# Kernel optimization log

Measured on AMD Instinct MI355X. Metric: run time of the kernel, lower is better.

## Reference

```python
import jax, jax.numpy as jnp
import numpy as np

ACT = jax.nn.relu
REG = 1.0  # semi_dual_sgd passes reg=1 (not self.e)
N_ITER = 1000


def _convt(x, w, b, out_pad):
    # PyTorch ConvTranspose2d, w layout [Cin, Cout, kh, kw], k=3, stride=2, padding=1
    wk = jnp.transpose(w[:, :, ::-1, ::-1], (1, 0, 2, 3))  # -> OIHW
    y = jax.lax.conv_general_dilated(
        x, wk, window_strides=(1, 1),
        padding=((1, 1 + out_pad), (1, 1 + out_pad)),
        lhs_dilation=(2, 2),
        dimension_numbers=("NCHW", "OIHW", "NCHW"))
    return y + b[None, :, None, None]


def _conv(x, w, b):
    # Conv2d k=3, padding=1, w layout OIHW
    y = jax.lax.conv_general_dilated(
        x, w, window_strides=(1, 1), padding=((1, 1), (1, 1)),
        dimension_numbers=("NCHW", "OIHW", "NCHW"))
    return y + b[None, :, None, None]


def _decoder_logits(z, fc_w, fc_b, ct0_w, ct0_b, ct1_w, ct1_b, fct_w, fct_b, conv_w, conv_b):
    h = ACT(z @ fc_w + fc_b)            # [n, 128*16]
    h = h.reshape(-1, 128, 4, 4)
    h = ACT(_convt(h, ct0_w, ct0_b, 0))  # [n, 64, 7, 7]  (img_size==28 branch: output_padding=0)
    h = ACT(_convt(h, ct1_w, ct1_b, 1))  # [n, 32, 14, 14]
    h = ACT(_convt(h, fct_w, fct_b, 1))  # [n, 32, 28, 28]
    return _conv(h, conv_w, conv_b)      # [n, 1, 28, 28] Bernoulli logits


def _cost_matrix(x, logit):
    # C[i,j] = -sum_pix Bernoulli(logits=logit_j).log_prob(x_i)
    # log_prob = x*logit - softplus(logit); sum over pixels factorizes into a GEMM.
    B = x.shape[0]
    n = logit.shape[0]
    X = x.reshape(B, -1)          # [B, P]
    L = logit.reshape(n, -1)      # [n, P]
    sp = jnp.sum(jax.nn.softplus(L), axis=1)  # [n]
    return -(X @ L.T) + sp[None, :]           # [B, n]


def _sag_semi_dual(C, idx, reg):
    # SAG on the semi-dual entropic OT objective (Genevay et al. / POT-style),
    # uniform marginals, lr = reg / max(a) = reg * n_src.
    n_src, n_tgt = C.shape
    a = jnp.full((n_src,), 1.0 / n_src, dtype=C.dtype)
    b = jnp.full((n_tgt,), 1.0 / n_tgt, dtype=C.dtype)
    log_b = jnp.log(b)
    lr = reg * n_src

    def step(carry, i):
        beta, stored, ssum = carry
        # stable softmax form of exp(-(C[i]-beta)/reg)*b / sum(...)
        khi = jax.nn.softmax((beta - C[i]) / reg + log_b)
        g = a[i] * (b - khi)
        ssum = ssum + g - stored[i]
        stored = stored.at[i].set(g)
        beta = beta + (lr / n_src) * ssum
        return (beta, stored, ssum), None

    init = (jnp.zeros((n_tgt,), C.dtype), jnp.zeros((n_src, n_tgt), C.dtype), jnp.zeros((n_tgt,), C.dtype))
    (beta, _, _), _ = jax.lax.scan(step, init, idx)

    # entropic c-transform and primal plan recovery
    alpha = -reg * jax.scipy.special.logsumexp((beta[None, :] - C) / reg + log_b[None, :], axis=1)
    P = jnp.exp((alpha[:, None] + beta[None, :] - C) / reg) * a[:, None] * b[None, :]
    return P, a, b


def _omega(x):
    xs = jnp.where(x <= 0.0, 1.0, x)
    return jnp.sum(xs * jnp.log(xs))


def setup_inputs() -> dict:
    key = jax.random.key(0)
    ks = jax.random.split(key, 16)
    B, N, LAT = 512, 512, 64
    s = 0.05
    return {
        "x": jax.random.uniform(ks[0], (B, 1, 28, 28), jnp.float32),
        "z": jax.random.normal(ks[1], (N, LAT), jnp.float32),
        "fc_w": jax.random.normal(ks[2], (LAT, 128 * 16), jnp.float32) * s,
        "fc_b": jnp.zeros((128 * 16,), jnp.float32),
        "ct0_w": jax.random.normal(ks[3], (128, 64, 3, 3), jnp.float32) * s,
        "ct0_b": jnp.zeros((64,), jnp.float32),
        "ct1_w": jax.random.normal(ks[4], (64, 32, 3, 3), jnp.float32) * s,
        "ct1_b": jnp.zeros((32,), jnp.float32),
        "fct_w": jax.random.normal(ks[5], (32, 32, 3, 3), jnp.float32) * s,
        "fct_b": jnp.zeros((32,), jnp.float32),
        "conv_w": jax.random.normal(ks[6], (1, 32, 3, 3), jnp.float32) * s,
        "conv_b": jnp.zeros((1,), jnp.float32),
        "idx": jax.random.randint(ks[7], (N_ITER,), 0, B, jnp.int32),
    }


def reference(x, z, fc_w, fc_b, ct0_w, ct0_b, ct1_w, ct1_b, fct_w, fct_b, conv_w, conv_b, idx):
    logit = _decoder_logits(z, fc_w, fc_b, ct0_w, ct0_b, ct1_w, ct1_b, fct_w, fct_b, conv_w, conv_b)
    C = _cost_matrix(x, logit)                 # [B, n_sample]
    P, px, pz = _sag_semi_dual(C, idx, REG)    # numItermax=1000, reg=1
    kl = _omega(P) - _omega(px) - _omega(pz)
    return (P, C, kl)
```

## Files before the change

### kernel.cpp

```cpp
#include <hip/hip_runtime.h>
#include <hip/hip_bf16.h>
#include <math.h>


typedef float vf4 __attribute__((ext_vector_type(4)));

__global__ void fc_relu_k(const float* __restrict__ z, const float* __restrict__ w,
                          const float* __restrict__ b, float* __restrict__ out) {
  int n = blockIdx.x >> 1;
  int c0 = ((blockIdx.x & 1) << 10) + threadIdx.x * 4;
  const float* zr = z + n * 64;
  float4 acc = *(const float4*)&b[c0];
#pragma unroll
  for (int k = 0; k < 64; ++k) {
    float zk = zr[k];
    float4 wv = *(const float4*)&w[k * 2048 + c0];
    acc.x = fmaf(zk, wv.x, acc.x);
    acc.y = fmaf(zk, wv.y, acc.y);
    acc.z = fmaf(zk, wv.z, acc.z);
    acc.w = fmaf(zk, wv.w, acc.w);
  }
  acc.x = fmaxf(acc.x, 0.f); acc.y = fmaxf(acc.y, 0.f);
  acc.z = fmaxf(acc.z, 0.f); acc.w = fmaxf(acc.w, 0.f);
  *(float4*)&out[n * 2048 + c0] = acc;
}

#define TAPF(T, P, XV) { \
  const float4* w4_ = reinterpret_cast<const float4*>(&wt[((T) * CIN + ci) * 8]); \
  float4 wa_ = w4_[0], wb_ = w4_[1]; \
  acc[P][0] = fmaf(XV, wa_.x, acc[P][0]); \
  acc[P][1] = fmaf(XV, wa_.y, acc[P][1]); \
  acc[P][2] = fmaf(XV, wa_.z, acc[P][2]); \
  acc[P][3] = fmaf(XV, wa_.w, acc[P][3]); \
  acc[P][4] = fmaf(XV, wb_.x, acc[P][4]); \
  acc[P][5] = fmaf(XV, wb_.y, acc[P][5]); \
  acc[P][6] = fmaf(XV, wb_.z, acc[P][6]); \
  acc[P][7] = fmaf(XV, wb_.w, acc[P][7]); }

template <int CIN, int COUT, int HIN, int HOUT>
__global__ void convt_quad_k(const float* __restrict__ x, const float* __restrict__ w,
                             const float* __restrict__ bias, float* __restrict__ y) {
  constexpr bool FULL = (HOUT == 2 * HIN);
  constexpr int QP = HIN * HIN;
  __shared__ float wt[9 * CIN * 8];
  const int tid = threadIdx.x;
  const int g8 = blockIdx.y * 8;
  for (int e = tid; e < 9 * CIN * 8; e += 256) {
    int cl = e & 7;
    int rest = e >> 3;
    int ci = rest & (CIN - 1);
    int t = rest / CIN;
    wt[e] = w[((size_t)ci * COUT + g8 + cl) * 9 + t];
  }
  __syncthreads();

  int q = blockIdx.x * 256 + tid;
  int n = q / QP;
  int pq = q % QP;
  int a = pq / HIN, b = pq % HIN;
  const bool oka = (a + 1 < HIN), okb = (b + 1 < HIN);
  const float* xim = x + (size_t)n * CIN * QP + a * HIN + b;

  float acc[4][8];
#pragma unroll
  for (int p = 0; p < 4; ++p)
#pragma unroll
    for (int c = 0; c < 8; ++c) acc[p][c] = 0.f;

  for (int ci = 0; ci < CIN; ++ci) {
    const float* xc = xim + ci * QP;
    float x00 = xc[0];
    float x01 = okb ? xc[1] : 0.f;
    float x10 = oka ? xc[HIN] : 0.f;
    float x11 = (oka && okb) ? xc[HIN + 1] : 0.f;
    TAPF(4, 0, x00)
    TAPF(3, 1, x01) TAPF(5, 1, x00)
    TAPF(1, 2, x10) TAPF(7, 2, x00)
    TAPF(0, 3, x11) TAPF(2, 3, x10) TAPF(6, 3, x01) TAPF(8, 3, x00)
  }

  int oh0 = 2 * a, ow0 = 2 * b;
  bool vh = FULL || (oh0 + 1 < HOUT);
  bool vw = FULL || (ow0 + 1 < HOUT);
#pragma unroll
  for (int c = 0; c < 8; ++c) {
    float bv = bias[g8 + c];
    float o00 = fmaxf(acc[0][c] + bv, 0.f);
    float o01 = fmaxf(acc[1][c] + bv, 0.f);
    float o10 = fmaxf(acc[2][c] + bv, 0.f);
    float o11 = fmaxf(acc[3][c] + bv, 0.f);
    float* yb = y + (((size_t)n * COUT + g8 + c) * HOUT + oh0) * (size_t)HOUT + ow0;
    if (FULL) {
      *(float2*)yb = make_float2(o00, o01);
      *(float2*)(yb + HOUT) = make_float2(o10, o11);
    } else {
      yb[0] = o00;
      if (vw) yb[1] = o01;
      if (vh) yb[HOUT] = o10;
      if (vh && vw) yb[HOUT + 1] = o11;
    }
  }
}

__global__ void conv_final_k(const float* __restrict__ x, const float* __restrict__ w,
                             const float* __restrict__ bias, float* __restrict__ y) {
  __shared__ float ws_[288];
  int tid = threadIdx.x;
  if (tid < 288) ws_[tid] = w[tid];
  __syncthreads();
  int gid = blockIdx.x * 256 + tid;
  int ow = gid % 28;
  int t1 = gid / 28;
  int oh = t1 % 28;
  int n = t1 / 28;
  bool h0 = oh > 0, h2 = oh < 27, w0 = ow > 0, w2 = ow < 27;
  const float* xb = x + (size_t)n * 32 * 784 + (oh - 1) * 28 + (ow - 1);
  float acc = bias[0];
  for (int ci = 0; ci < 32; ++ci) {
    const float* xc = xb + ci * 784;
    const float* wc = &ws_[ci * 9];
    if (h0 && w0) acc = fmaf(xc[0], wc[0], acc);
    if (h0)       acc = fmaf(xc[1], wc[1], acc);
    if (h0 && w2) acc = fmaf(xc[2], wc[2], acc);
    if (w0)       acc = fmaf(xc[28], wc[3], acc);
                  acc = fmaf(xc[29], wc[4], acc);
    if (w2)       acc = fmaf(xc[30], wc[5], acc);
    if (h2 && w0) acc = fmaf(xc[56], wc[6], acc);
    if (h2)       acc = fmaf(xc[57], wc[7], acc);
    if (h2 && w2) acc = fmaf(xc[58], wc[8], acc);
  }
  y[gid] = acc;
}

template <int CTRL>
__device__ __forceinline__ float dpp_f(float x) {
  return __int_as_float(__builtin_amdgcn_update_dpp(0, __float_as_int(x), CTRL, 0xF, 0xF, true));
}
__device__ __forceinline__ float rdl(float v, int l) {
  return __int_as_float(__builtin_amdgcn_readlane(__float_as_int(v), l));
}
__device__ __forceinline__ float wsum64_l63(float v) {
  v += dpp_f<0xB1>(v);
  v += dpp_f<0x4E>(v);
  v += dpp_f<0x141>(v);
  v += dpp_f<0x140>(v);
  v += dpp_f<0x142>(v);
  v += dpp_f<0x143>(v);
  return rdl(v, 63);
}
__device__ __forceinline__ float wmax64_l63(float v) {
  v = fmaxf(v, dpp_f<0xB1>(v));
  v = fmaxf(v, dpp_f<0x4E>(v));
  v = fmaxf(v, dpp_f<0x141>(v));
  v = fmaxf(v, dpp_f<0x140>(v));
  v = fmaxf(v, dpp_f<0x142>(v));
  v = fmaxf(v, dpp_f<0x143>(v));
  return rdl(v, 63);
}

__global__ void cost_k(const float* __restrict__ X, const float* __restrict__ L,
                       float* __restrict__ Craw, float* __restrict__ sp) {
  __shared__ float Xs[16][36];
  __shared__ float Ls[16][68];
  int tid = threadIdx.x;
  int i0 = blockIdx.y * 32, j0 = blockIdx.x * 64;
  int lrow = tid >> 2;
  int lq = tid & 3;
  int xrow = tid & 31;
  int xq = (tid >> 5) & 3;
  bool doX = tid < 128;
  bool doSP = (blockIdx.y == 0);
  int tx = tid & 15, ty = tid >> 4;
  float acc[2][4] = {};
  float spacc = 0.f;
  for (int k0 = 0; k0 < 784; k0 += 16) {
    float4 lv = *(const float4*)&L[(size_t)(j0 + lrow) * 784 + k0 + lq * 4];
    float4 xv = {0.f, 0.f, 0.f, 0.f};
    if (doX) xv = *(const float4*)&X[(size_t)(i0 + xrow) * 784 + k0 + xq * 4];
    __syncthreads();
    Ls[lq * 4 + 0][lrow] = lv.x; Ls[lq * 4 + 1][lrow] = lv.y;
    Ls[lq * 4 + 2][lrow] = lv.z; Ls[lq * 4 + 3][lrow] = lv.w;
    if (doX) {
      Xs[xq * 4 + 0][xrow] = xv.x; Xs[xq * 4 + 1][xrow] = xv.y;
      Xs[xq * 4 + 2][xrow] = xv.z; Xs[xq * 4 + 3][xrow] = xv.w;
    }
    if (doSP) {
      spacc += fmaxf(lv.x, 0.f) + log1pf(__expf(-fabsf(lv.x)));
      spacc += fmaxf(lv.y, 0.f) + log1pf(__expf(-fabsf(lv.y)));
      spacc += fmaxf(lv.z, 0.f) + log1pf(__expf(-fabsf(lv.z)));
      spacc += fmaxf(lv.w, 0.f) + log1pf(__expf(-fabsf(lv.w)));
    }
    __syncthreads();
#pragma unroll
    for (int k = 0; k < 16; ++k) {
      float2 a = *(const float2*)&Xs[k][ty * 2];
      float4 bq = *(const float4*)&Ls[k][tx * 4];
      acc[0][0] = fmaf(a.x, bq.x, acc[0][0]); acc[0][1] = fmaf(a.x, bq.y, acc[0][1]);
      acc[0][2] = fmaf(a.x, bq.z, acc[0][2]); acc[0][3] = fmaf(a.x, bq.w, acc[0][3]);
      acc[1][0] = fmaf(a.y, bq.x, acc[1][0]); acc[1][1] = fmaf(a.y, bq.y, acc[1][1]);
      acc[1][2] = fmaf(a.y, bq.z, acc[1][2]); acc[1][3] = fmaf(a.y, bq.w, acc[1][3]);
    }
  }
#pragma unroll
  for (int r = 0; r < 2; ++r) {
    float4 o = make_float4(acc[r][0], acc[r][1], acc[r][2], acc[r][3]);
    *(float4*)&Craw[(size_t)(i0 + ty * 2 + r) * 512 + j0 + tx * 4] = o;
  }
  if (doSP) {
    float q = spacc;
    q += dpp_f<0xB1>(q);
    q += dpp_f<0x4E>(q);
    if (lq == 0) sp[j0 + lrow] = q;
  }
}

__global__ void prep_k(const float* __restrict__ craw, const float* __restrict__ sp,
                       float* __restrict__ D2) {
  __shared__ float red[256];
  int i = blockIdx.x, tid = threadIdx.x;
  float c0 = craw[(size_t)i * 512 + tid];
  float c1 = craw[(size_t)i * 512 + tid + 256];
  float v0 = c0 - sp[tid];
  float v1 = c1 - sp[tid + 256];
  red[tid] = fmaxf(v0, v1);
  __syncthreads();
  for (int st = 128; st > 0; st >>= 1) {
    if (tid < st) red[tid] = fmaxf(red[tid], red[tid + st]);
    __syncthreads();
  }
  float m = red[0];
  const float L2E = 1.4426950408889634f;
  D2[(size_t)i * 512 + tid] = (m - v0) * L2E;
  D2[(size_t)i * 512 + tid + 256] = (m - v1) * L2E;
}

#define SLD0(ROW) { const float* cp_ = D2 + ((size_t)(unsigned)(ROW) << 9) + jb; \
  s0dA = *(const vf4*)cp_; s0dB = *(const vf4*)(cp_ + 4); \
  const float* tp_ = stored + ((size_t)(unsigned)(ROW) << 9) + jb; \
  s0sA = *(const vf4*)tp_; s0sB = *(const vf4*)(tp_ + 4); }
#define SLD1(ROW) { const float* cp_ = D2 + ((size_t)(unsigned)(ROW) << 9) + jb; \
  s1dA = *(const vf4*)cp_; s1dB = *(const vf4*)(cp_ + 4); \
  const float* tp_ = stored + ((size_t)(unsigned)(ROW) << 9) + jb; \
  s1sA = *(const vf4*)tp_; s1sB = *(const vf4*)(tp_ + 4); }

#define STEP(RR, PFR, DA, DB, SA, SB, LDM, \
             R1,A1,B1, R2,A2,B2, R3,A3,B3, R4,A4,B4, R5,A5,B5, R6,A6,B6, \
             GA, GB) \
{ \
  vf4 d0_ = DA, d1_ = DB, t0_ = SA, t1_ = SB; \
  LDM(PFR); \
  const int r_ = (RR); \
  if (__builtin_expect((r_==(R1)) | (r_==(R2)) | (r_==(R3)) | \
                       (r_==(R4)) | (r_==(R5)) | (r_==(R6)), 0)) { \
    if (r_==(R6)) { t0_ = A6; t1_ = B6; } \
    if (r_==(R5)) { t0_ = A5; t1_ = B5; } \
    if (r_==(R4)) { t0_ = A4; t1_ = B4; } \
    if (r_==(R3)) { t0_ = A3; t1_ = B3; } \
    if (r_==(R2)) { t0_ = A2; t1_ = B2; } \
    if (r_==(R1)) { t0_ = A1; t1_ = B1; } \
  } \
  vf4 u0_ = ssumL - t0_; \
  vf4 u1_ = ssumH - t1_; \
  vf4 a0_ = betaL - d0_; \
  vf4 a1_ = betaH - d1_; \
  vf4 e0_, e1_; \
  e0_.x = __builtin_amdgcn_exp2f(a0_.x); e0_.y = __builtin_amdgcn_exp2f(a0_.y); \
  e0_.z = __builtin_amdgcn_exp2f(a0_.z); e0_.w = __builtin_amdgcn_exp2f(a0_.w); \
  e1_.x = __builtin_amdgcn_exp2f(a1_.x); e1_.y = __builtin_amdgcn_exp2f(a1_.y); \
  e1_.z = __builtin_amdgcn_exp2f(a1_.z); e1_.w = __builtin_amdgcn_exp2f(a1_.w); \
  vf4 es_ = e0_ + e1_; \
  float S_ = wsum64_l63((es_.x + es_.z) + (es_.y + es_.w)); \
  S_ = fmaxf(S_, 1e-35f); \
  float kk_ = C2NL * __builtin_amdgcn_rcpf(S_); \
  vf4 g0_ = e0_ * kk_ + c1l4; \
  vf4 g1_ = e1_ * kk_ + c1l4; \
  ssumL = u0_ + g0_; ssumH = u1_ + g1_; \
  betaL += ssumL; betaH += ssumH; \
  float* wp_ = stored + ((size_t)(unsigned)r_ << 9) + jb; \
  *(vf4*)wp_ = g0_; *(vf4*)(wp_ + 4) = g1_; \
  GA = g0_; GB = g1_; \
}

__global__ void __launch_bounds__(512, 1) sag_k(const float* __restrict__ D2,
                                                const int* __restrict__ idx,
                                                float* __restrict__ stored,
                                                float* __restrict__ beta_out) {
  const int tid = threadIdx.x;
  if (tid >= 64) {
    const vf4* c4 = (const vf4*)D2;
    const vf4* s4 = (const vf4*)stored;
    vf4 acc = {0.f, 0.f, 0.f, 0.f};
    for (int p = tid - 64; p < 65536; p += 448) { acc += c4[p]; acc += s4[p]; }
    float accs = acc.x + acc.y + acc.z + acc.w;
    asm volatile("" :: "v"(accs));
    return;
  }

  const int jb = tid * 8;
  const float C2NL = -0.0028177637f;
  const vf4 c1l4 = {5.503574e-06f, 5.503574e-06f, 5.503574e-06f, 5.503574e-06f};

  vf4 z4 = {0.f, 0.f, 0.f, 0.f};
  vf4 betaL = z4, betaH = z4, ssumL = z4, ssumH = z4;
  vf4 h1A = z4, h1B = z4, h2A = z4, h2B = z4, h3A = z4, h3B = z4;
  vf4 h4A = z4, h4B = z4, h5A = z4, h5B = z4, h6A = z4, h6B = z4;
  int hr1 = -1, hr2 = -1, hr3 = -1, hr4 = -1, hr5 = -1, hr6 = -1;
  float vsh = 0.f;

  int4 ia = *(const int4*)&idx[0];
  int4 ib = *(const int4*)&idx[4];
  int i0 = ia.x, i1 = ia.y, i2 = ia.z, i3 = ia.w;
  int i4 = ib.x, i5 = ib.y, i6 = ib.z, i7 = ib.w;

  vf4 s0dA, s0dB, s0sA, s0sB, s1dA, s1dB, s1sA, s1sB;
  SLD0(i0);
  SLD1(i1);

  vf4 g0a, g0b, g1a, g1b, g2a, g2b, g3a, g3b;
  vf4 g4a, g4b, g5a, g5b, g6a, g6b, g7a, g7b;

  for (int t = 0; t < 1000; t += 8) {
    int tb = (t + 8 < 1000) ? (t + 8) : 992;
    int4 na = *(const int4*)&idx[tb];
    int4 nb = *(const int4*)&idx[tb + 4];

    STEP(i0, i2, s0dA, s0dB, s0sA, s0sB, SLD0,
         hr1,h1A,h1B, hr2,h2A,h2B, hr3,h3A,h3B, hr4,h4A,h4B, hr5,h5A,h5B, hr6,h6A,h6B,
         g0a, g0b)
    STEP(i1, i3, s1dA, s1dB, s1sA, s1sB, SLD1,
         i0,g0a,g0b, hr1,h1A,h1B, hr2,h2A,h2B, hr3,h3A,h3B, hr4,h4A,h4B, hr5,h5A,h5B,
         g1a, g1b)
    STEP(i2, i4, s0dA, s0dB, s0sA, s0sB, SLD0,
         i1,g1a,g1b, i0,g0a,g0b, hr1,h1A,h1B, hr2,h2A,h2B, hr3,h3A,h3B, hr4,h4A,h4B,
         g2a, g2b)
    STEP(i3, i5, s1dA, s1dB, s1sA, s1sB, SLD1,
         i2,g2a,g2b, i1,g1a,g1b, i0,g0a,g0b, hr1,h1A,h1B, hr2,h2A,h2B, hr3,h3A,h3B,
         g3a, g3b)
    STEP(i4, i6, s0dA, s0dB, s0sA, s0sB, SLD0,
         i3,g3a,g3b, i2,g2a,g2b, i1,g1a,g1b, i0,g0a,g0b, hr1,h1A,h1B, hr2,h2A,h2B,
         g4a, g4b)
    STEP(i5, i7, s1dA, s1dB, s1sA, s1sB, SLD1,
         i4,g4a,g4b, i3,g3a,g3b, i2,g2a,g2b, i1,g1a,g1b, i0,g0a,g0b, hr1,h1A,h1B,
         g5a, g5b)
    STEP(i6, na.x, s0dA, s0dB, s0sA, s0sB, SLD0,
         i5,g5a,g5b, i4,g4a,g4b, i3,g3a,g3b, i2,g2a,g2b, i1,g1a,g1b, i0,g0a,g0b,
         g6a, g6b)
    STEP(i7, na.y, s1dA, s1dB, s1sA, s1sB, SLD1,
         i6,g6a,g6b, i5,g5a,g5b, i4,g4a,g4b, i3,g3a,g3b, i2,g2a,g2b, i1,g1a,g1b,
         g7a, g7b)

    {
      vf4 qm;
      qm.x = fmaxf(betaL.x, betaH.x); qm.y = fmaxf(betaL.y, betaH.y);
      qm.z = fmaxf(betaL.z, betaH.z); qm.w = fmaxf(betaL.w, betaH.w);
      float lm = fmaxf(fmaxf(qm.x, qm.y), fmaxf(qm.z, qm.w));
      float dm = wmax64_l63(lm);
      betaL = betaL - dm; betaH = betaH - dm;
      vsh += dm;
    }

    hr1 = i7; h1A = g7a; h1B = g7b;
    hr2 = i6; h2A = g6a; h2B = g6b;
    hr3 = i5; h3A = g5a; h3B = g5b;
    hr4 = i4; h4A = g4a; h4B = g4b;
    hr5 = i3; h5A = g3a; h5B = g3b;
    hr6 = i2; h6A = g2a; h6B = g2b;
    i0 = na.x; i1 = na.y; i2 = na.z; i3 = na.w;
    i4 = nb.x; i5 = nb.y; i6 = nb.z; i7 = nb.w;
  }

  const float LN2 = 0.6931471805599453f;
  vf4 oL = (betaL + vsh) * LN2;
  vf4 oH = (betaH + vsh) * LN2;
  *(vf4*)(beta_out + jb) = oL;
  *(vf4*)(beta_out + jb + 4) = oH;
}

__global__ void p_k(const float* __restrict__ craw, const float* __restrict__ sp,
                    const float* __restrict__ beta, float* __restrict__ P,
                    float* __restrict__ Cout, float* __restrict__ rowsum) {
  __shared__ float red[256];
  int i = blockIdx.x, tid = threadIdx.x;
  float c0 = craw[(size_t)i * 512 + tid];
  float c1 = craw[(size_t)i * 512 + tid + 256];
  float sp0 = sp[tid], sp1 = sp[tid + 256];
  float u0 = (beta[tid] - sp0) + c0;
  float u1 = (beta[tid + 256] - sp1) + c1;
  Cout[(size_t)i * 512 + tid] = sp0 - c0;
  Cout[(size_t)i * 512 + tid + 256] = sp1 - c1;
  float m = fmaxf(u0, u1);
  red[tid] = m;
  __syncthreads();
  for (int st = 128; st > 0; st >>= 1) {
    if (tid < st) red[tid] = fmaxf(red[tid], red[tid + st]);
    __syncthreads();
  }
  m = red[0];
  __syncthreads();
  float e0 = __expf(u0 - m), e1 = __expf(u1 - m);
  red[tid] = e0 + e1;
  __syncthreads();
  for (int st = 128; st > 0; st >>= 1) {
    if (tid < st) red[tid] += red[tid + st];
    __syncthreads();
  }
  float lse = m + logf(red[0]);
  __syncthreads();
  const float log512 = 6.238324625039508f;
  float p0 = __expf(u0 - lse) * (1.0f / 512.0f);
  float p1 = __expf(u1 - lse) * (1.0f / 512.0f);
  P[(size_t)i * 512 + tid] = p0;
  P[(size_t)i * 512 + tid + 256] = p1;
  float pl = p0 * (u0 - lse - log512) + p1 * (u1 - lse - log512);
  red[tid] = pl;
  __syncthreads();
  for (int st = 128; st > 0; st >>= 1) {
    if (tid < st) red[tid] += red[tid + st];
    __syncthreads();
  }
  if (tid == 0) rowsum[i] = red[0];
}

__global__ void kl_k(const float* __restrict__ rowsum, float* __restrict__ out_kl) {
  __shared__ float red[512];
  int tid = threadIdx.x;
  red[tid] = rowsum[tid];
  __syncthreads();
  for (int st = 256; st > 0; st >>= 1) {
    if (tid < st) red[tid] += red[tid + st];
    __syncthreads();
  }
  if (tid == 0) out_kl[0] = red[0] + 2.0f * 6.238324625039508f;
}

extern "C" void kernel_launch(void* const* d_in, const int* in_sizes, int n_in,
                              void* d_out, int out_size, void* d_ws, size_t ws_size,
                              hipStream_t stream) {
  const float* x = (const float*)d_in[0];
  const float* z = (const float*)d_in[1];
  const float* fc_w = (const float*)d_in[2];
  const float* fc_b = (const float*)d_in[3];
  const float* ct0_w = (const float*)d_in[4];
  const float* ct0_b = (const float*)d_in[5];
  const float* ct1_w = (const float*)d_in[6];
  const float* ct1_b = (const float*)d_in[7];
  const float* fct_w = (const float*)d_in[8];
  const float* fct_b = (const float*)d_in[9];
  const float* conv_w = (const float*)d_in[10];
  const float* conv_b = (const float*)d_in[11];
  const int* idx = (const int*)d_in[12];

  float* out = (float*)d_out;
  float* Pout = out;
  float* Cout = out + 262144;
  float* klout = out + 524288;

  float* ws = (float*)d_ws;
  float* h0 = ws;
  float* h1 = h0 + 1048576;
  float* h2 = h1 + 1605632;
  float* h3 = h2 + 3211264;
  float* logit = h3 + 12845056;
  float* sp = logit + 401408;
  float* beta = sp + 512;
  float* stored = beta + 512;
  float* rowsum = stored + 262144;
  float* Craw = h0;
  float* D2 = h1;

  hipMemsetAsync(stored, 0, 262144 * sizeof(float), stream);

  fc_relu_k<<<1024, 256, 0, stream>>>(z, fc_w, fc_b, h0);
  convt_quad_k<128, 64, 4, 7><<<dim3(32, 8), 256, 0, stream>>>(h0, ct0_w, ct0_b, h1);
  convt_quad_k<64, 32, 7, 14><<<dim3(98, 4), 256, 0, stream>>>(h1, ct1_w, ct1_b, h2);
  convt_quad_k<32, 32, 14, 28><<<dim3(392, 4), 256, 0, stream>>>(h2, fct_w, fct_b, h3);
  conv_final_k<<<1568, 256, 0, stream>>>(h3, conv_w, conv_b, logit);
  cost_k<<<dim3(8, 16), 256, 0, stream>>>(x, logit, Craw, sp);
  prep_k<<<512, 256, 0, stream>>>(Craw, sp, D2);
  sag_k<<<1, 512, 0, stream>>>(D2, idx, stored, beta);
  p_k<<<512, 256, 0, stream>>>(Craw, sp, beta, Pout, Cout, rowsum);
  kl_k<<<1, 512, 0, stream>>>(rowsum, klout);
}
```

Measured before the change: 540.3 us.

## Split SAG loop across eight waves, one column per lane, LDS reduction

```diff
diff --git a/kernel.cpp b/kernel.cpp
--- a/kernel.cpp
+++ b/kernel.cpp
@@ -234,146 +234,107 @@
   D2[(size_t)i * 512 + tid + 256] = (m - v1) * L2E;
 }
 
-#define SLD0(ROW) { const float* cp_ = D2 + ((size_t)(unsigned)(ROW) << 9) + jb; \
-  s0dA = *(const vf4*)cp_; s0dB = *(const vf4*)(cp_ + 4); \
-  const float* tp_ = stored + ((size_t)(unsigned)(ROW) << 9) + jb; \
-  s0sA = *(const vf4*)tp_; s0sB = *(const vf4*)(tp_ + 4); }
-#define SLD1(ROW) { const float* cp_ = D2 + ((size_t)(unsigned)(ROW) << 9) + jb; \
-  s1dA = *(const vf4*)cp_; s1dB = *(const vf4*)(cp_ + 4); \
-  const float* tp_ = stored + ((size_t)(unsigned)(ROW) << 9) + jb; \
-  s1sA = *(const vf4*)tp_; s1sB = *(const vf4*)(tp_ + 4); }
-
-#define STEP(RR, PFR, DA, DB, SA, SB, LDM, \
-             R1,A1,B1, R2,A2,B2, R3,A3,B3, R4,A4,B4, R5,A5,B5, R6,A6,B6, \
-             GA, GB) \
+#define SPF(SLOTD, SLOTS, ROW) { unsigned ro_ = (unsigned)(ROW); \
+  SLOTD = D2[((size_t)ro_ << 9) + col]; \
+  SLOTS = stored[((size_t)ro_ << 9) + col]; }
+
+#define SSTEP(RR, PFR, SD, SS, PAR, R1,G1, R2,G2, R3,G3, R4,G4, R5,G5, R6,G6, GOUT) \
 { \
-  vf4 d0_ = DA, d1_ = DB, t0_ = SA, t1_ = SB; \
-  LDM(PFR); \
+  float d_ = SD, st_ = SS; \
+  SPF(SD, SS, PFR) \
   const int r_ = (RR); \
   if (__builtin_expect((r_==(R1)) | (r_==(R2)) | (r_==(R3)) | \
                        (r_==(R4)) | (r_==(R5)) | (r_==(R6)), 0)) { \
-    if (r_==(R6)) { t0_ = A6; t1_ = B6; } \
-    if (r_==(R5)) { t0_ = A5; t1_ = B5; } \
-    if (r_==(R4)) { t0_ = A4; t1_ = B4; } \
-    if (r_==(R3)) { t0_ = A3; t1_ = B3; } \
-    if (r_==(R2)) { t0_ = A2; t1_ = B2; } \
-    if (r_==(R1)) { t0_ = A1; t1_ = B1; } \
+    if (r_==(R6)) st_ = G6; \
+    if (r_==(R5)) st_ = G5; \
+    if (r_==(R4)) st_ = G4; \
+    if (r_==(R3)) st_ = G3; \
+    if (r_==(R2)) st_ = G2; \
+    if (r_==(R1)) st_ = G1; \
   } \
-  vf4 u0_ = ssumL - t0_; \
-  vf4 u1_ = ssumH - t1_; \
-  vf4 a0_ = betaL - d0_; \
-  vf4 a1_ = betaH - d1_; \
-  vf4 e0_, e1_; \
-  e0_.x = __builtin_amdgcn_exp2f(a0_.x); e0_.y = __builtin_amdgcn_exp2f(a0_.y); \
-  e0_.z = __builtin_amdgcn_exp2f(a0_.z); e0_.w = __builtin_amdgcn_exp2f(a0_.w); \
-  e1_.x = __builtin_amdgcn_exp2f(a1_.x); e1_.y = __builtin_amdgcn_exp2f(a1_.y); \
-  e1_.z = __builtin_amdgcn_exp2f(a1_.z); e1_.w = __builtin_amdgcn_exp2f(a1_.w); \
-  vf4 es_ = e0_ + e1_; \
-  float S_ = wsum64_l63((es_.x + es_.z) + (es_.y + es_.w)); \
+  float e_ = __builtin_amdgcn_exp2f(beta - d_); \
+  float part_ = wsum64_l63(e_); \
+  if (lane == 63) sdata[(PAR) * 8 + wid] = part_; \
+  __syncthreads(); \
+  vf4 qa_ = *(const vf4*)&sdata[(PAR) * 8]; \
+  vf4 qb_ = *(const vf4*)&sdata[(PAR) * 8 + 4]; \
+  float S_ = ((qa_.x + qa_.y) + (qa_.z + qa_.w)) + ((qb_.x + qb_.y) + (qb_.z + qb_.w)); \
   S_ = fmaxf(S_, 1e-35f); \
   float kk_ = C2NL * __builtin_amdgcn_rcpf(S_); \
-  vf4 g0_ = e0_ * kk_ + c1l4; \
-  vf4 g1_ = e1_ * kk_ + c1l4; \
-  ssumL = u0_ + g0_; ssumH = u1_ + g1_; \
-  betaL += ssumL; betaH += ssumH; \
-  float* wp_ = stored + ((size_t)(unsigned)r_ << 9) + jb; \
-  *(vf4*)wp_ = g0_; *(vf4*)(wp_ + 4) = g1_; \
-  GA = g0_; GB = g1_; \
+  float g_ = e_ * kk_ + c1l4; \
+  ssum += g_ - st_; \
+  beta += ssum; \
+  stored[((size_t)(unsigned)r_ << 9) + col] = g_; \
+  GOUT = g_; \
 }
 
 __global__ void __launch_bounds__(512, 1) sag_k(const float* __restrict__ D2,
                                                 const int* __restrict__ idx,
                                                 float* __restrict__ stored,
                                                 float* __restrict__ beta_out) {
+  __shared__ __align__(16) float sdata[24];
   const int tid = threadIdx.x;
-  if (tid >= 64) {
-    const vf4* c4 = (const vf4*)D2;
-    const vf4* s4 = (const vf4*)stored;
-    vf4 acc = {0.f, 0.f, 0.f, 0.f};
-    for (int p = tid - 64; p < 65536; p += 448) { acc += c4[p]; acc += s4[p]; }
-    float accs = acc.x + acc.y + acc.z + acc.w;
-    asm volatile("" :: "v"(accs));
-    return;
-  }
-
-  const int jb = tid * 8;
+  const int wid = tid >> 6;
+  const int lane = tid & 63;
+  const int col = (wid << 6) + lane;
   const float C2NL = -0.0028177637f;
-  const vf4 c1l4 = {5.503574e-06f, 5.503574e-06f, 5.503574e-06f, 5.503574e-06f};
-
-  vf4 z4 = {0.f, 0.f, 0.f, 0.f};
-  vf4 betaL = z4, betaH = z4, ssumL = z4, ssumH = z4;
-  vf4 h1A = z4, h1B = z4, h2A = z4, h2B = z4, h3A = z4, h3B = z4;
-  vf4 h4A = z4, h4B = z4, h5A = z4, h5B = z4, h6A = z4, h6B = z4;
+  const float c1l4 = 5.503574e-06f;
+
+  float beta = 0.f, ssum = 0.f, vsh = 0.f;
+  float h1 = 0.f, h2 = 0.f, h3 = 0.f, h4 = 0.f, h5 = 0.f, h6 = 0.f;
   int hr1 = -1, hr2 = -1, hr3 = -1, hr4 = -1, hr5 = -1, hr6 = -1;
-  float vsh = 0.f;
 
   int4 ia = *(const int4*)&idx[0];
   int4 ib = *(const int4*)&idx[4];
   int i0 = ia.x, i1 = ia.y, i2 = ia.z, i3 = ia.w;
   int i4 = ib.x, i5 = ib.y, i6 = ib.z, i7 = ib.w;
 
-  vf4 s0dA, s0dB, s0sA, s0sB, s1dA, s1dB, s1sA, s1sB;
-  SLD0(i0);
-  SLD1(i1);
-
-  vf4 g0a, g0b, g1a, g1b, g2a, g2b, g3a, g3b;
-  vf4 g4a, g4b, g5a, g5b, g6a, g6b, g7a, g7b;
+  float sd0, sd1, sd2, sd3, ss0, ss1, ss2, ss3;
+  SPF(sd0, ss0, i0)
+  SPF(sd1, ss1, i1)
+  SPF(sd2, ss2, i2)
+  SPF(sd3, ss3, i3)
+
+  float g0, g1, g2, g3, g4, g5, g6, g7;
 
   for (int t = 0; t < 1000; t += 8) {
     int tb = (t + 8 < 1000) ? (t + 8) : 992;
     int4 na = *(const int4*)&idx[tb];
     int4 nb = *(const int4*)&idx[tb + 4];
 
-    STEP(i0, i2, s0dA, s0dB, s0sA, s0sB, SLD0,
-         hr1,h1A,h1B, hr2,h2A,h2B, hr3,h3A,h3B, hr4,h4A,h4B, hr5,h5A,h5B, hr6,h6A,h6B,
-         g0a, g0b)
-    STEP(i1, i3, s1dA, s1dB, s1sA, s1sB, SLD1,
-         i0,g0a,g0b, hr1,h1A,h1B, hr2,h2A,h2B, hr3,h3A,h3B, hr4,h4A,h4B, hr5,h5A,h5B,
-         g1a, g1b)
-    STEP(i2, i4, s0dA, s0dB, s0sA, s0sB, SLD0,
-         i1,g1a,g1b, i0,g0a,g0b, hr1,h1A,h1B, hr2,h2A,h2B, hr3,h3A,h3B, hr4,h4A,h4B,
-         g2a, g2b)
-    STEP(i3, i5, s1dA, s1dB, s1sA, s1sB, SLD1,
-         i2,g2a,g2b, i1,g1a,g1b, i0,g0a,g0b, hr1,h1A,h1B, hr2,h2A,h2B, hr3,h3A,h3B,
-         g3a, g3b)
-    STEP(i4, i6, s0dA, s0dB, s0sA, s0sB, SLD0,
-         i3,g3a,g3b, i2,g2a,g2b, i1,g1a,g1b, i0,g0a,g0b, hr1,h1A,h1B, hr2,h2A,h2B,
-         g4a, g4b)
-    STEP(i5, i7, s1dA, s1dB, s1sA, s1sB, SLD1,
-         i4,g4a,g4b, i3,g3a,g3b, i2,g2a,g2b, i1,g1a,g1b, i0,g0a,g0b, hr1,h1A,h1B,
-         g5a, g5b)
-    STEP(i6, na.x, s0dA, s0dB, s0sA, s0sB, SLD0,
-         i5,g5a,g5b, i4,g4a,g4b, i3,g3a,g3b, i2,g2a,g2b, i1,g1a,g1b, i0,g0a,g0b,
-         g6a, g6b)
-    STEP(i7, na.y, s1dA, s1dB, s1sA, s1sB, SLD1,
-         i6,g6a,g6b, i5,g5a,g5b, i4,g4a,g4b, i3,g3a,g3b, i2,g2a,g2b, i1,g1a,g1b,
-         g7a, g7b)
+    SSTEP(i0, i4,   sd0, ss0, 0, hr1,h1, hr2,h2, hr3,h3, hr4,h4, hr5,h5, hr6,h6, g0)
+    SSTEP(i1, i5,   sd1, ss1, 1, i0,g0, hr1,h1, hr2,h2, hr3,h3, hr4,h4, hr5,h5, g1)
+    SSTEP(i2, i6,   sd2, ss2, 0, i1,g1, i0,g0, hr1,h1, hr2,h2, hr3,h3, hr4,h4, g2)
+    SSTEP(i3, i7,   sd3, ss3, 1, i2,g2, i1,g1, i0,g0, hr1,h1, hr2,h2, hr3,h3, g3)
+    SSTEP(i4, na.x, sd0, ss0, 0, i3,g3, i2,g2, i1,g1, i0,g0, hr1,h1, hr2,h2, g4)
+    SSTEP(i5, na.y, sd1, ss1, 1, i4,g4, i3,g3, i2,g2, i1,g1, i0,g0, hr1,h1, g5)
+    SSTEP(i6, na.z, sd2, ss2, 0, i5,g5, i4,g4, i3,g3, i2,g2, i1,g1, i0,g0, g6)
+    SSTEP(i7, na.w, sd3, ss3, 1, i6,g6, i5,g5, i4,g4, i3,g3, i2,g2, i1,g1, g7)
 
     {
-      vf4 qm;
-      qm.x = fmaxf(betaL.x, betaH.x); qm.y = fmaxf(betaL.y, betaH.y);
-      qm.z = fmaxf(betaL.z, betaH.z); qm.w = fmaxf(betaL.w, betaH.w);
-      float lm = fmaxf(fmaxf(qm.x, qm.y), fmaxf(qm.z, qm.w));
-      float dm = wmax64_l63(lm);
-      betaL = betaL - dm; betaH = betaH - dm;
+      float bm = wmax64_l63(beta);
+      if (lane == 63) sdata[16 + wid] = bm;
+      __syncthreads();
+      vf4 qa = *(const vf4*)&sdata[16];
+      vf4 qb = *(const vf4*)&sdata[20];
+      float dm = fmaxf(fmaxf(fmaxf(qa.x, qa.y), fmaxf(qa.z, qa.w)),
+                       fmaxf(fmaxf(qb.x, qb.y), fmaxf(qb.z, qb.w)));
+      beta -= dm;
       vsh += dm;
     }
 
-    hr1 = i7; h1A = g7a; h1B = g7b;
-    hr2 = i6; h2A = g6a; h2B = g6b;
-    hr3 = i5; h3A = g5a; h3B = g5b;
-    hr4 = i4; h4A = g4a; h4B = g4b;
-    hr5 = i3; h5A = g3a; h5B = g3b;
-    hr6 = i2; h6A = g2a; h6B = g2b;
+    hr1 = i7; h1 = g7;
+    hr2 = i6; h2 = g6;
+    hr3 = i5; h3 = g5;
+    hr4 = i4; h4 = g4;
+    hr5 = i3; h5 = g3;
+    hr6 = i2; h6 = g2;
     i0 = na.x; i1 = na.y; i2 = na.z; i3 = na.w;
     i4 = nb.x; i5 = nb.y; i6 = nb.z; i7 = nb.w;
   }
 
   const float LN2 = 0.6931471805599453f;
-  vf4 oL = (betaL + vsh) * LN2;
-  vf4 oH = (betaH + vsh) * LN2;
-  *(vf4*)(beta_out + jb) = oL;
-  *(vf4*)(beta_out + jb + 4) = oH;
+  beta_out[col] = (beta + vsh) * LN2;
 }
 
 __global__ void p_k(const float* __restrict__ craw, const float* __restrict__ sp,
```

After: 648.1 us. 19.9% more time.
